# Kernel optimization log

Measured on AMD Instinct MI355X. Metric: run time of the kernel, lower is better.

The kernel has to match this reference:

```python
import jax, jax.numpy as jnp
import numpy as np

B, T, K = 256, 512, 128
LR_MULT = 1.0  # learning_rate_multiplier


def setup_inputs() -> dict:
    key = jax.random.key(0)
    k1, k2, k3 = jax.random.split(key, 3)
    emissions = jax.random.normal(k1, (B, T, K), dtype=jnp.float32)
    mask = jax.random.randint(k2, (B, T), 0, 2, dtype=jnp.int32)
    # learned CRF transition matrix (stand-in for Orthogonal init)
    transition_weight = jax.random.normal(k3, (K, K), dtype=jnp.float32)
    return {"emissions": emissions, "mask": mask, "transition_weight": transition_weight}


def reference(emissions, mask, transition_weight):
    # Viterbi decode (tfa.text.crf_decode semantics): sequence_lengths = sum(mask),
    # state frozen for steps t >= length, output tags multiplied by mask.
    mask = mask.astype(jnp.int32)
    lengths = jnp.sum(mask, axis=1)                       # [B]
    trans = transition_weight * LR_MULT                   # [K,K]
    Tn = emissions.shape[1]

    init_state = emissions[:, 0, :]                       # [B,K] viterbi scores at t=0
    ts = jnp.arange(1, Tn)                                # steps 1..T-1
    em_rest = jnp.swapaxes(emissions[:, 1:, :], 0, 1)     # [T-1,B,K]

    def fwd_step(state, inp):
        e_t, t = inp                                      # e_t: [B,K]
        scores = state[:, :, None] + trans[None, :, :]    # [B, K_prev, K_cur]
        bp = jnp.argmax(scores, axis=1).astype(jnp.int32)  # [B,K] best prev tag
        new_state = jnp.max(scores, axis=1) + e_t         # [B,K]
        valid = (t < lengths)[:, None]                    # step valid iff t <= len-1
        return jnp.where(valid, new_state, state), bp

    last_state, bps = jax.lax.scan(fwd_step, init_state, (em_rest, ts))  # bps: [T-1,B,K]
    last_tag = jnp.argmax(last_state, axis=1).astype(jnp.int32)  # tag at pos length-1

    def bwd_step(tag, inp):
        bp_t, t = inp                                     # bp_t: [B,K]
        prev = jnp.take_along_axis(bp_t, tag[:, None], axis=1)[:, 0]
        tag = jnp.where(t < lengths, prev, tag)           # carry tag beyond seq end
        return tag, tag

    # reverse scan: ys[i] = tag at position i, for positions 0..T-2
    _, tags_prefix = jax.lax.scan(bwd_step, last_tag, (bps, ts), reverse=True)
    tags = jnp.concatenate([jnp.swapaxes(tags_prefix, 0, 1), last_tag[:, None]], axis=1)
    return tags * mask
```

## Files before the change

kernel.cpp:

```cpp
#include <hip/hip_runtime.h>

#define NB 256
#define NT 512
#define NK 128
#define GRP 8

__device__ __forceinline__ void upd(float v, int i, float& bv, int& bi) {
    bool g = v > bv;
    bv = g ? v : bv;
    bi = g ? i : bi;
}

__global__ __launch_bounds__(256, 1)
void crf_decode_kernel(const float* __restrict__ em,
                       const int* __restrict__ mask,
                       const float* __restrict__ trans,
                       int* __restrict__ out) {
    __shared__ alignas(16) float state_sh[2][NK];
    __shared__ unsigned char bp_sh[(NT - 1) * NK];
    __shared__ int tags_sh[NT];
    __shared__ int len_sh, lt_sh;

    const int b    = blockIdx.x;
    const int tid  = threadIdx.x;
    const int l    = tid & 63;
    const int w    = tid >> 6;
    const int jj   = (w << 5) | (l & 31);
    const int half = l >> 5;
    const long base = (long)b * NT * NK;

    int s = mask[b * NT + tid] + mask[b * NT + tid + 256];
    #pragma unroll
    for (int off = 32; off > 0; off >>= 1) s += __shfl_down(s, off, 64);
    if (tid == 0) len_sh = 0;
    __syncthreads();
    if (l == 0) atomicAdd(&len_sh, s);

    float treg[64];
    #pragma unroll
    for (int ii = 0; ii < 64; ++ii)
        treg[ii] = trans[(half * 64 + ii) * NK + jj];

    if (half == 0) state_sh[0][jj] = em[base + jj];
    __syncthreads();
    const int len = len_sh;

    int cur = 0;
    int t = 1;

    float ld[GRP];
    #pragma unroll
    for (int k = 0; k < GRP; ++k) {
        int tt = t + k; tt = tt < NT ? tt : NT - 1;
        ld[k] = em[base + tt * NK + jj];
    }

    auto step = [&](int tt, float e) {
        const float4* sp = (const float4*)&state_sh[cur][half * 64];
        float bv0 = -3.4e38f, bv1 = -3.4e38f, bv2 = -3.4e38f, bv3 = -3.4e38f;
        int bi0 = half*64 + 0, bi1 = half*64 + 1, bi2 = half*64 + 2, bi3 = half*64 + 3;
        #pragma unroll
        for (int g = 0; g < 16; ++g) {
            float4 sv = sp[g];
            const int ib = half * 64 + 4 * g;
            upd(sv.x + treg[4*g + 0], ib + 0, bv0, bi0);
            upd(sv.y + treg[4*g + 1], ib + 1, bv1, bi1);
            upd(sv.z + treg[4*g + 2], ib + 2, bv2, bi2);
            upd(sv.w + treg[4*g + 3], ib + 3, bv3, bi3);
        }
        bool tk;
        tk = (bv1 > bv0) || (bv1 == bv0 && bi1 < bi0);
        float mv0 = tk ? bv1 : bv0; int mi0 = tk ? bi1 : bi0;
        tk = (bv3 > bv2) || (bv3 == bv2 && bi3 < bi2);
        float mv1 = tk ? bv3 : bv2; int mi1 = tk ? bi3 : bi2;
        tk = (mv1 > mv0) || (mv1 == mv0 && mi1 < mi0);
        float bv = tk ? mv1 : mv0;  int bi = tk ? mi1 : mi0;

        float vo = __shfl_xor(bv, 32, 64);
        int   io = __shfl_xor(bi, 32, 64);
        bool t2 = (vo > bv) || (vo == bv && io < bi);
        float fv = t2 ? vo : bv;
        int   fi = t2 ? io : bi;

        if (half == 0) state_sh[cur ^ 1][jj] = fv + e;
        else           bp_sh[(tt - 1) * NK + jj] = (unsigned char)fi;
        __syncthreads();
        cur ^= 1;
    };

    while (t + GRP <= len) {
        float ec[GRP];
        #pragma unroll
        for (int k = 0; k < GRP; ++k) ec[k] = ld[k];
        #pragma unroll
        for (int k = 0; k < GRP; ++k) {
            int tt = t + GRP + k; tt = tt < NT ? tt : NT - 1;
            ld[k] = em[base + tt * NK + jj];
        }
        #pragma unroll
        for (int k = 0; k < GRP; ++k) step(t + k, ec[k]);
        t += GRP;
    }
    for (; t < len; ++t) {
        float e = em[base + t * NK + jj];
        step(t, e);
    }

    if (tid < 64) {
        float v0 = state_sh[cur][tid], v1 = state_sh[cur][tid + 64];
        bool take = v1 > v0;
        float v = take ? v1 : v0;
        int  ix = take ? tid + 64 : tid;
        #pragma unroll
        for (int off = 32; off > 0; off >>= 1) {
            float vo = __shfl_xor(v, off, 64);
            int   io = __shfl_xor(ix, off, 64);
            bool t2 = (vo > v) || (vo == v && io < ix);
            v  = t2 ? vo : v;
            ix = t2 ? io : ix;
        }
        if (tid == 0) lt_sh = ix;
    }
    __syncthreads();
    const int last_tag = lt_sh;
    const int lm1 = (len > 0) ? (len - 1) : 0;

    for (int p = tid; p < NT; p += 256)
        if (p >= lm1) tags_sh[p] = last_tag;
    __syncthreads();

    if (tid == 0) {
        int tag = last_tag;
        for (int p = lm1 - 1; p >= 0; --p) {
            tag = (int)bp_sh[p * NK + tag];
            tags_sh[p] = tag;
        }
    }
    __syncthreads();

    for (int p = tid; p < NT; p += 256) {
        int mv = mask[b * NT + p];
        out[b * NT + p] = mv ? tags_sh[p] : 0;
    }
}

extern "C" void kernel_launch(void* const* d_in, const int* in_sizes, int n_in,
                              void* d_out, int out_size, void* d_ws, size_t ws_size,
                              hipStream_t stream) {
    const float* em    = (const float*)d_in[0];
    const int*   mask  = (const int*)d_in[1];
    const float* trans = (const float*)d_in[2];
    int* out = (int*)d_out;
    hipLaunchKernelGGL(crf_decode_kernel, dim3(NB), dim3(256), 0, stream,
                       em, mask, trans, out);
}
```

Baseline: 379.0 us.

## Use lighter LDS-only barrier in forward loop and wave-parallel readlane backtrace

Replaces __syncthreads in the Viterbi forward step with an inline s_waitcnt lgkmcnt(0) plus s_barrier, so each step no longer waits on outstanding global prefetch loads (vmcnt). The serial single-thread backtrace becomes a full wave that preloads backpointer rows into registers in blocks of 8 steps and chases tags with readlane, which avoids a dependent LDS load per step. It also uses fmaxf in the max update. Skipping the vmcnt wait depends on the inline asm being correct about which memory operations have to finish, and a readlane with a lane index that varies per step may compile to a waterfall loop.

```diff
diff --git a/kernel.cpp b/kernel.cpp
--- a/kernel.cpp
+++ b/kernel.cpp
@@ -5,9 +5,14 @@
 #define NK 128
 #define GRP 8
 
+#define WAVE_BARRIER() do {                                            \
+    asm volatile("s_waitcnt lgkmcnt(0)\n\ts_barrier" ::: "memory");    \
+    __builtin_amdgcn_sched_barrier(0);                                 \
+} while (0)
+
 __device__ __forceinline__ void upd(float v, int i, float& bv, int& bi) {
     bool g = v > bv;
-    bv = g ? v : bv;
+    bv = fmaxf(v, bv);
     bi = g ? i : bi;
 }
 
@@ -17,7 +22,7 @@
                        const float* __restrict__ trans,
                        int* __restrict__ out) {
     __shared__ alignas(16) float state_sh[2][NK];
-    __shared__ unsigned char bp_sh[(NT - 1) * NK];
+    __shared__ alignas(16) unsigned char bp_sh[(NT - 1) * NK];
     __shared__ int tags_sh[NT];
     __shared__ int len_sh, lt_sh;
 
@@ -84,7 +89,7 @@
 
         if (half == 0) state_sh[cur ^ 1][jj] = fv + e;
         else           bp_sh[(tt - 1) * NK + jj] = (unsigned char)fi;
-        __syncthreads();
+        WAVE_BARRIER();
         cur ^= 1;
     };
 
@@ -129,11 +134,60 @@
         if (p >= lm1) tags_sh[p] = last_tag;
     __syncthreads();
 
-    if (tid == 0) {
+    if (tid < 64) {
+        const unsigned int* bpw = (const unsigned int*)bp_sh;
         int tag = last_tag;
-        for (int p = lm1 - 1; p >= 0; --p) {
+        int p = lm1 - 1;
+        while (p >= 0 && ((p + 1) & 7)) {
             tag = (int)bp_sh[p * NK + tag];
-            tags_sh[p] = tag;
+            if (l == 0) tags_sh[p] = tag;
+            --p;
+        }
+        if (p >= 7) {
+            int cb = p - 7;
+            unsigned int cur0, cur1, cur2, cur3;
+            cur0 = bpw[(cb + 0 + (l >> 5)) * 32 + (l & 31)];
+            cur1 = bpw[(cb + 2 + (l >> 5)) * 32 + (l & 31)];
+            cur2 = bpw[(cb + 4 + (l >> 5)) * 32 + (l & 31)];
+            cur3 = bpw[(cb + 6 + (l >> 5)) * 32 + (l & 31)];
+            while (true) {
+                const int nb = cb - 8;
+                unsigned int nxt0 = 0, nxt1 = 0, nxt2 = 0, nxt3 = 0;
+                if (nb >= 0) {
+                    nxt0 = bpw[(nb + 0 + (l >> 5)) * 32 + (l & 31)];
+                    nxt1 = bpw[(nb + 2 + (l >> 5)) * 32 + (l & 31)];
+                    nxt2 = bpw[(nb + 4 + (l >> 5)) * 32 + (l & 31)];
+                    nxt3 = bpw[(nb + 6 + (l >> 5)) * 32 + (l & 31)];
+                }
+                unsigned int wd;
+                wd = __builtin_amdgcn_readlane(cur3, 32 + (tag >> 2));
+                tag = (int)((wd >> ((tag & 3) * 8)) & 0xFF);
+                if (l == 0) tags_sh[cb + 7] = tag;
+                wd = __builtin_amdgcn_readlane(cur3, (tag >> 2));
+                tag = (int)((wd >> ((tag & 3) * 8)) & 0xFF);
+                if (l == 0) tags_sh[cb + 6] = tag;
+                wd = __builtin_amdgcn_readlane(cur2, 32 + (tag >> 2));
+                tag = (int)((wd >> ((tag & 3) * 8)) & 0xFF);
+                if (l == 0) tags_sh[cb + 5] = tag;
+                wd = __builtin_amdgcn_readlane(cur2, (tag >> 2));
+                tag = (int)((wd >> ((tag & 3) * 8)) & 0xFF);
+                if (l == 0) tags_sh[cb + 4] = tag;
+                wd = __builtin_amdgcn_readlane(cur1, 32 + (tag >> 2));
+                tag = (int)((wd >> ((tag & 3) * 8)) & 0xFF);
+                if (l == 0) tags_sh[cb + 3] = tag;
+                wd = __builtin_amdgcn_readlane(cur1, (tag >> 2));
+                tag = (int)((wd >> ((tag & 3) * 8)) & 0xFF);
+                if (l == 0) tags_sh[cb + 2] = tag;
+                wd = __builtin_amdgcn_readlane(cur0, 32 + (tag >> 2));
+                tag = (int)((wd >> ((tag & 3) * 8)) & 0xFF);
+                if (l == 0) tags_sh[cb + 1] = tag;
+                wd = __builtin_amdgcn_readlane(cur0, (tag >> 2));
+                tag = (int)((wd >> ((tag & 3) * 8)) & 0xFF);
+                if (l == 0) tags_sh[cb + 0] = tag;
+                if (nb < 0) break;
+                cur0 = nxt0; cur1 = nxt1; cur2 = nxt2; cur3 = nxt3;
+                cb = nb;
+            }
         }
     }
     __syncthreads();
```

After: 335.1 us. -11.6%, faster.
